# Performance work log

Measured on AMD Instinct MI355X. Metric: run time of the kernel, lower is better.

The kernel has to match this reference:

```python
import jax, jax.numpy as jnp
import numpy as np

H = 64  # hidden_size hardcoded in the module


def _lstm_scan(x_pre, w_hh):
    # x_pre: [T, B, 4H] = x @ W_ih^T + b_ih + b_hh, precomputed for all steps
    # w_hh: [4H, H]. PyTorch gate order: i, f, g, o.
    B = x_pre.shape[1]
    h0 = jnp.zeros((B, H), x_pre.dtype)
    c0 = jnp.zeros((B, H), x_pre.dtype)

    def cell(carry, xp):
        h, c = carry
        gates = xp + h @ w_hh.T  # [B, 4H]
        i, f, g, o = jnp.split(gates, 4, axis=-1)
        i = jax.nn.sigmoid(i)
        f = jax.nn.sigmoid(f)
        g = jnp.tanh(g)
        o = jax.nn.sigmoid(o)
        c = f * c + i * g
        h = o * jnp.tanh(c)
        return (h, c), h

    _, hs = jax.lax.scan(cell, (h0, c0), x_pre)
    return hs  # [T, B, H]


def _bidir_layer(x, w_ih, w_hh, b_ih, b_hh):
    # x: [T, B, D]; w_ih: [2, 4H, D]; w_hh: [2, 4H, H]; b_*: [2, 4H]
    pre_f = jnp.einsum('tbd,gd->tbg', x, w_ih[0]) + b_ih[0] + b_hh[0]
    hs_f = _lstm_scan(pre_f, w_hh[0])
    xr = x[::-1]
    pre_b = jnp.einsum('tbd,gd->tbg', xr, w_ih[1]) + b_ih[1] + b_hh[1]
    hs_b = _lstm_scan(pre_b, w_hh[1])[::-1]  # re-reverse to align with time
    return jnp.concatenate([hs_f, hs_b], axis=-1)  # [T, B, 2H]


def setup_inputs() -> dict:
    key = jax.random.key(0)
    B, T, F = 1024, 512, 32
    ks = jax.random.split(key, 11)
    s = 1.0 / float(np.sqrt(H))  # PyTorch LSTM init: U(-1/sqrt(H), 1/sqrt(H))
    u = lambda k, shape: jax.random.uniform(k, shape, jnp.float32, -s, s)
    return dict(
        x=jax.random.normal(ks[0], (B, T, F), jnp.float32),
        w_ih0=u(ks[1], (2, 4 * H, F)),
        w_hh0=u(ks[2], (2, 4 * H, H)),
        b_ih0=u(ks[3], (2, 4 * H)),
        b_hh0=u(ks[4], (2, 4 * H)),
        w_ih1=u(ks[5], (2, 4 * H, 2 * H)),
        w_hh1=u(ks[6], (2, 4 * H, H)),
        b_ih1=u(ks[7], (2, 4 * H)),
        b_hh1=u(ks[8], (2, 4 * H)),
        fc_w=u(ks[9], (2, 2 * H)),
        fc_b=u(ks[10], (2,)),
    )


def reference(x, w_ih0, w_hh0, b_ih0, b_hh0, w_ih1, w_hh1, b_ih1, b_hh1, fc_w, fc_b):
    xt = jnp.transpose(x, (1, 0, 2))  # [T, B, F]
    h1 = _bidir_layer(xt, w_ih0, w_hh0, b_ih0, b_hh0)  # [T, B, 2H]
    h2 = _bidir_layer(h1, w_ih1, w_hh1, b_ih1, b_hh1)  # [T, B, 2H]
    last = h2[-1]  # out[:, -1, :] in batch_first layout -> [B, 2H]
    return last @ fc_w.T + fc_b  # [B, 2]
```

## Files before the change

kernel.cpp:

```cpp
#include <hip/hip_runtime.h>

#define TT 512
#define BB 1024
#define FF 32
#define HH 64
#define GG 256

__device__ float g_h1[(size_t)BB * TT * 2 * HH];
__device__ float g_pre0[(size_t)2 * BB * TT * GG];
__device__ float g_pre1[(size_t)BB * TT * GG];
__device__ float g_hf[(size_t)BB * HH];

__device__ __forceinline__ float fsigm(float x) {
    float e = __builtin_amdgcn_exp2f(x * -1.44269504088896f);
    return __builtin_amdgcn_rcpf(1.0f + e);
}
__device__ __forceinline__ float ftanh(float x) {
    float e = __builtin_amdgcn_exp2f(x * -2.88539008177793f);
    return 2.0f * __builtin_amdgcn_rcpf(1.0f + e) - 1.0f;
}
__device__ __forceinline__ float rlane(float v, int l) {
    return __int_as_float(__builtin_amdgcn_readlane(__float_as_int(v), l));
}

#define FMA4(c, s, b) do { c.x += (s)*(b).x; c.y += (s)*(b).y; \
                           c.z += (s)*(b).z; c.w += (s)*(b).w; } while (0)

__global__ __launch_bounds__(256, 4) void pre_gemm0(
    const float* __restrict__ x,
    const float* __restrict__ w_ih,
    const float* __restrict__ b_ih,
    const float* __restrict__ b_hh)
{
    const int tid = threadIdx.x;
    const int b   = blockIdx.x >> 1;
    const int dir = blockIdx.x & 1;

    const float4* wsrc = (const float4*)(w_ih + ((size_t)dir * GG + tid) * FF);
    const float4 w0 = wsrc[0], w1 = wsrc[1], w2 = wsrc[2], w3 = wsrc[3],
                 w4 = wsrc[4], w5 = wsrc[5], w6 = wsrc[6], w7 = wsrc[7];
    const float bias = b_ih[dir * GG + tid] + b_hh[dir * GG + tid];

    const float* xb = x + (size_t)b * TT * FF;
    float* ob = g_pre0 + ((size_t)(dir * BB + b) * TT) * GG + tid;

#pragma unroll 2
    for (int t = 0; t < TT; ++t) {
        const float* xp = xb + t * FF;
        float a = bias;
        a += xp[0]  * w0.x + xp[1]  * w0.y + xp[2]  * w0.z + xp[3]  * w0.w;
        a += xp[4]  * w1.x + xp[5]  * w1.y + xp[6]  * w1.z + xp[7]  * w1.w;
        a += xp[8]  * w2.x + xp[9]  * w2.y + xp[10] * w2.z + xp[11] * w2.w;
        a += xp[12] * w3.x + xp[13] * w3.y + xp[14] * w3.z + xp[15] * w3.w;
        a += xp[16] * w4.x + xp[17] * w4.y + xp[18] * w4.z + xp[19] * w4.w;
        a += xp[20] * w5.x + xp[21] * w5.y + xp[22] * w5.z + xp[23] * w5.w;
        a += xp[24] * w6.x + xp[25] * w6.y + xp[26] * w6.z + xp[27] * w6.w;
        a += xp[28] * w7.x + xp[29] * w7.y + xp[30] * w7.z + xp[31] * w7.w;
        ob[(size_t)t * GG] = a;
    }
}

#define PINQ(wq) \
    asm volatile("" : "+v"(wq.x), "+v"(wq.y), "+v"(wq.z), "+v"(wq.w))

template <int L>
__global__ __launch_bounds__(64, 1) void lstm_scan(
    const float* __restrict__ w_hh)
{
    const int l   = threadIdx.x;
    const int dir = (L == 0) ? (blockIdx.x & 1) : 0;
    const int b   = (L == 0) ? (int)(blockIdx.x >> 1) : (int)blockIdx.x;

    const float* wbase = w_hh + (size_t)dir * GG * HH;

    const float4* pi_ = (const float4*)(wbase + (size_t)(0  + l) * HH);
    const float4* pf_ = (const float4*)(wbase + (size_t)(64 + l) * HH);
    float4 wi0 = pi_[0],  wi1 = pi_[1],  wi2 = pi_[2],  wi3 = pi_[3],
           wi4 = pi_[4],  wi5 = pi_[5],  wi6 = pi_[6],  wi7 = pi_[7],
           wi8 = pi_[8],  wi9 = pi_[9],  wi10 = pi_[10], wi11 = pi_[11],
           wi12 = pi_[12], wi13 = pi_[13], wi14 = pi_[14], wi15 = pi_[15];
    float4 wf0 = pf_[0],  wf1 = pf_[1],  wf2 = pf_[2],  wf3 = pf_[3],
           wf4 = pf_[4],  wf5 = pf_[5],  wf6 = pf_[6],  wf7 = pf_[7],
           wf8 = pf_[8],  wf9 = pf_[9],  wf10 = pf_[10], wf11 = pf_[11],
           wf12 = pf_[12], wf13 = pf_[13], wf14 = pf_[14], wf15 = pf_[15];
    PINQ(wi0);  PINQ(wi1);  PINQ(wi2);  PINQ(wi3);
    PINQ(wi4);  PINQ(wi5);  PINQ(wi6);  PINQ(wi7);
    PINQ(wi8);  PINQ(wi9);  PINQ(wi10); PINQ(wi11);
    PINQ(wi12); PINQ(wi13); PINQ(wi14); PINQ(wi15);
    PINQ(wf0);  PINQ(wf1);  PINQ(wf2);  PINQ(wf3);
    PINQ(wf4);  PINQ(wf5);  PINQ(wf6);  PINQ(wf7);
    PINQ(wf8);  PINQ(wf9);  PINQ(wf10); PINQ(wf11);
    PINQ(wf12); PINQ(wf13); PINQ(wf14); PINQ(wf15);

    float4 wg[16], wo[16];
    {
        const float4* pg_ = (const float4*)(wbase + (size_t)(128 + l) * HH);
        const float4* po_ = (const float4*)(wbase + (size_t)(192 + l) * HH);
#pragma unroll
        for (int q = 0; q < 16; ++q) { wg[q] = pg_[q]; wo[q] = po_[q]; }
    }

    const float* pre = (L == 0)
        ? (g_pre0 + ((size_t)(dir * BB + b)) * TT * GG)
        : (g_pre1 + (size_t)b * TT * GG);

    float c = 0.f, h = 0.f;

    const int t0 = dir ? (TT - 1) : 0;
    const int t1 = dir ? (TT - 2) : 1;
    const float* pp0 = pre + (size_t)t0 * GG;
    const float* pp1 = pre + (size_t)t1 * GG;
    float ci0 = pp0[l], cf0 = pp0[64 + l], cg0 = pp0[128 + l], co0 = pp0[192 + l];
    float ci1 = pp1[l], cf1 = pp1[64 + l], cg1 = pp1[128 + l], co1 = pp1[192 + l];

    for (int s = 0; s < TT; ++s) {
        const int t = dir ? (TT - 1 - s) : s;

        float ni = 0.f, nf = 0.f, ng = 0.f, no_ = 0.f;
        if (s + 2 < TT) {
            const int tn = dir ? (TT - 3 - s) : (s + 2);
            const float* np = pre + (size_t)tn * GG;
            ni = np[l]; nf = np[64 + l]; ng = np[128 + l]; no_ = np[192 + l];
        }

        float ai = ci0, af = cf0, ag = cg0, ao = co0;

#define STEPQ(q) do {                                                        \
        float s0 = rlane(h, 4*q+0), s1 = rlane(h, 4*q+1),                    \
              s2 = rlane(h, 4*q+2), s3 = rlane(h, 4*q+3);                    \
        ai += s0*wi##q.x + s1*wi##q.y + s2*wi##q.z + s3*wi##q.w;             \
        af += s0*wf##q.x + s1*wf##q.y + s2*wf##q.z + s3*wf##q.w;             \
        ag += s0*wg[q].x + s1*wg[q].y + s2*wg[q].z + s3*wg[q].w;             \
        ao += s0*wo[q].x + s1*wo[q].y + s2*wo[q].z + s3*wo[q].w;             \
    } while (0)

        STEPQ(0);  STEPQ(1);  STEPQ(2);  STEPQ(3);
        STEPQ(4);  STEPQ(5);  STEPQ(6);  STEPQ(7);
        STEPQ(8);  STEPQ(9);  STEPQ(10); STEPQ(11);
        STEPQ(12); STEPQ(13); STEPQ(14); STEPQ(15);
#undef STEPQ

        const float ig = fsigm(ai);
        const float fg = fsigm(af);
        const float gg = ftanh(ag);
        const float og = fsigm(ao);
        c = fg * c + ig * gg;
        h = og * ftanh(c);

        if (L == 0) {
            g_h1[((size_t)b * TT + t) * (2 * HH) + dir * HH + l] = h;
        } else {
            if (s == TT - 1) g_hf[(size_t)b * HH + l] = h;
        }

        ci0 = ci1; cf0 = cf1; cg0 = cg1; co0 = co1;
        ci1 = ni;  cf1 = nf;  cg1 = ng;  co1 = no_;
    }
}

__global__ __launch_bounds__(256, 2) void pre_gemm1(
    const float* __restrict__ w_ih,
    const float* __restrict__ b_ih,
    const float* __restrict__ b_hh)
{
    __shared__ __align__(16) float As[64 * 132];
    __shared__ __align__(16) float Bs[128 * 68];

    const int tid   = threadIdx.x;
    const int mbase = (int)(blockIdx.x >> 2) * 64;
    const int n0    = (int)(blockIdx.x & 3) * 64;

#pragma unroll
    for (int i = 0; i < 8; ++i) {
        const int qid = tid + 256 * i;
        const int r = qid >> 5, q = qid & 31;
        float4 v = *(const float4*)(g_h1 + (size_t)(mbase + r) * 128 + q * 4);
        *(float4*)(&As[r * 132 + q * 4]) = v;
    }
#pragma unroll
    for (int i = 0; i < 8; ++i) {
        const int qid = tid + 256 * i;
        const int r = qid >> 5, q = qid & 31;
        float4 v = *(const float4*)(w_ih + (size_t)(n0 + r) * 128 + q * 4);
        Bs[(q * 4 + 0) * 68 + r] = v.x;
        Bs[(q * 4 + 1) * 68 + r] = v.y;
        Bs[(q * 4 + 2) * 68 + r] = v.z;
        Bs[(q * 4 + 3) * 68 + r] = v.w;
    }
    __syncthreads();

    const int tx = tid & 15, ty = tid >> 4;

    float4 c0 = make_float4(0.f, 0.f, 0.f, 0.f);
    float4 c1 = c0, c2 = c0, c3 = c0;

#pragma unroll 8
    for (int kq = 0; kq < 32; ++kq) {
        const float4 a0 = *(const float4*)&As[(ty * 4 + 0) * 132 + kq * 4];
        const float4 a1 = *(const float4*)&As[(ty * 4 + 1) * 132 + kq * 4];
        const float4 a2 = *(const float4*)&As[(ty * 4 + 2) * 132 + kq * 4];
        const float4 a3 = *(const float4*)&As[(ty * 4 + 3) * 132 + kq * 4];
        const float4 b0 = *(const float4*)&Bs[(kq * 4 + 0) * 68 + tx * 4];
        const float4 b1 = *(const float4*)&Bs[(kq * 4 + 1) * 68 + tx * 4];
        const float4 b2 = *(const float4*)&Bs[(kq * 4 + 2) * 68 + tx * 4];
        const float4 b3 = *(const float4*)&Bs[(kq * 4 + 3) * 68 + tx * 4];
        FMA4(c0, a0.x, b0); FMA4(c0, a0.y, b1); FMA4(c0, a0.z, b2); FMA4(c0, a0.w, b3);
        FMA4(c1, a1.x, b0); FMA4(c1, a1.y, b1); FMA4(c1, a1.z, b2); FMA4(c1, a1.w, b3);
        FMA4(c2, a2.x, b0); FMA4(c2, a2.y, b1); FMA4(c2, a2.z, b2); FMA4(c2, a2.w, b3);
        FMA4(c3, a3.x, b0); FMA4(c3, a3.y, b1); FMA4(c3, a3.z, b2); FMA4(c3, a3.w, b3);
    }

    float4 bias4;
    bias4.x = b_ih[n0 + tx * 4 + 0] + b_hh[n0 + tx * 4 + 0];
    bias4.y = b_ih[n0 + tx * 4 + 1] + b_hh[n0 + tx * 4 + 1];
    bias4.z = b_ih[n0 + tx * 4 + 2] + b_hh[n0 + tx * 4 + 2];
    bias4.w = b_ih[n0 + tx * 4 + 3] + b_hh[n0 + tx * 4 + 3];

    FMA4(c0, 1.f, bias4); FMA4(c1, 1.f, bias4);
    FMA4(c2, 1.f, bias4); FMA4(c3, 1.f, bias4);

    float* ob = g_pre1 + (size_t)(mbase + ty * 4) * GG + n0 + tx * 4;
    *(float4*)(ob + 0 * (size_t)GG) = c0;
    *(float4*)(ob + 1 * (size_t)GG) = c1;
    *(float4*)(ob + 2 * (size_t)GG) = c2;
    *(float4*)(ob + 3 * (size_t)GG) = c3;
}

#define FMAC4(W, P0, P1, P2, P3, K) do{                                   \
    float4 v_;                                                           \
    v_ = (P0)[K]; acc0 += W.x*v_.x; acc0 += W.y*v_.y; acc0 += W.z*v_.z; acc0 += W.w*v_.w; \
    v_ = (P1)[K]; acc1 += W.x*v_.x; acc1 += W.y*v_.y; acc1 += W.z*v_.z; acc1 += W.w*v_.w; \
    v_ = (P2)[K]; acc2 += W.x*v_.x; acc2 += W.y*v_.y; acc2 += W.z*v_.z; acc2 += W.w*v_.w; \
    v_ = (P3)[K]; acc3 += W.x*v_.x; acc3 += W.y*v_.y; acc3 += W.z*v_.z; acc3 += W.w*v_.w; \
}while(0)

__global__ __launch_bounds__(256, 2) void lstm_final(
    const float* __restrict__ w_ih,
    const float* __restrict__ b_ih,
    const float* __restrict__ b_hh,
    const float* __restrict__ fc_w,
    const float* __restrict__ fc_b,
    float* __restrict__ out)
{
    const int tid = threadIdx.x;
    const int b0  = blockIdx.x * 4;

    __shared__ __align__(16) float x_lds[4][128];
    __shared__ __align__(16) float gact[4][GG];
    __shared__ __align__(16) float last[4][128];

#pragma unroll
    for (int r = 0; r < 2; ++r) {
        int idx = tid + r * 256;
        int b = idx >> 7, col = idx & 127;
        x_lds[b][col] = g_h1[((size_t)(b0 + b) * TT + (TT - 1)) * 128 + col];
    }

    const float4* p = (const float4*)(w_ih + ((size_t)GG + tid) * 128);
    float4 w0 = p[0],  w1 = p[1],  w2 = p[2],  w3 = p[3],  w4 = p[4],  w5 = p[5],
           w6 = p[6],  w7 = p[7],  w8 = p[8],  w9 = p[9],  w10 = p[10], w11 = p[11],
           w12 = p[12], w13 = p[13], w14 = p[14], w15 = p[15], w16 = p[16], w17 = p[17],
           w18 = p[18], w19 = p[19], w20 = p[20], w21 = p[21], w22 = p[22], w23 = p[23],
           w24 = p[24], w25 = p[25], w26 = p[26], w27 = p[27], w28 = p[28], w29 = p[29],
           w30 = p[30], w31 = p[31];
    const float bias = b_ih[GG + tid] + b_hh[GG + tid];
    __syncthreads();

    const float4* xb0 = (const float4*)x_lds[0];
    const float4* xb1 = (const float4*)x_lds[1];
    const float4* xb2 = (const float4*)x_lds[2];
    const float4* xb3 = (const float4*)x_lds[3];

    float acc0 = bias, acc1 = bias, acc2 = bias, acc3 = bias;
    FMAC4(w0, xb0, xb1, xb2, xb3, 0);   FMAC4(w1, xb0, xb1, xb2, xb3, 1);
    FMAC4(w2, xb0, xb1, xb2, xb3, 2);   FMAC4(w3, xb0, xb1, xb2, xb3, 3);
    FMAC4(w4, xb0, xb1, xb2, xb3, 4);   FMAC4(w5, xb0, xb1, xb2, xb3, 5);
    FMAC4(w6, xb0, xb1, xb2, xb3, 6);   FMAC4(w7, xb0, xb1, xb2, xb3, 7);
    FMAC4(w8, xb0, xb1, xb2, xb3, 8);   FMAC4(w9, xb0, xb1, xb2, xb3, 9);
    FMAC4(w10, xb0, xb1, xb2, xb3, 10); FMAC4(w11, xb0, xb1, xb2, xb3, 11);
    FMAC4(w12, xb0, xb1, xb2, xb3, 12); FMAC4(w13, xb0, xb1, xb2, xb3, 13);
    FMAC4(w14, xb0, xb1, xb2, xb3, 14); FMAC4(w15, xb0, xb1, xb2, xb3, 15);
    FMAC4(w16, xb0, xb1, xb2, xb3, 16); FMAC4(w17, xb0, xb1, xb2, xb3, 17);
    FMAC4(w18, xb0, xb1, xb2, xb3, 18); FMAC4(w19, xb0, xb1, xb2, xb3, 19);
    FMAC4(w20, xb0, xb1, xb2, xb3, 20); FMAC4(w21, xb0, xb1, xb2, xb3, 21);
    FMAC4(w22, xb0, xb1, xb2, xb3, 22); FMAC4(w23, xb0, xb1, xb2, xb3, 23);
    FMAC4(w24, xb0, xb1, xb2, xb3, 24); FMAC4(w25, xb0, xb1, xb2, xb3, 25);
    FMAC4(w26, xb0, xb1, xb2, xb3, 26); FMAC4(w27, xb0, xb1, xb2, xb3, 27);
    FMAC4(w28, xb0, xb1, xb2, xb3, 28); FMAC4(w29, xb0, xb1, xb2, xb3, 29);
    FMAC4(w30, xb0, xb1, xb2, xb3, 30); FMAC4(w31, xb0, xb1, xb2, xb3, 31);

    const bool is_g = ((tid >> 6) == 2);
    gact[0][tid] = is_g ? ftanh(acc0) : fsigm(acc0);
    gact[1][tid] = is_g ? ftanh(acc1) : fsigm(acc1);
    gact[2][tid] = is_g ? ftanh(acc2) : fsigm(acc2);
    gact[3][tid] = is_g ? ftanh(acc3) : fsigm(acc3);
    __syncthreads();

    {
        const int cb = tid >> 6, cj = tid & 63;
        float ig = gact[cb][cj];
        float gg = gact[cb][2 * HH + cj];
        float og = gact[cb][3 * HH + cj];
        float c = ig * gg;
        float h = og * ftanh(c);
        last[cb][HH + cj] = h;
        last[cb][cj] = g_hf[(size_t)(b0 + cb) * HH + cj];
    }
    __syncthreads();

    if (tid < 8) {
        int b = tid >> 1, o = tid & 1;
        float a = fc_b[o];
#pragma unroll
        for (int j = 0; j < 128; ++j) a += fc_w[o * 128 + j] * last[b][j];
        out[(size_t)(b0 + b) * 2 + o] = a;
    }
}

extern "C" void kernel_launch(void* const* d_in, const int* in_sizes, int n_in,
                              void* d_out, int out_size, void* d_ws, size_t ws_size,
                              hipStream_t stream) {
    const float* x     = (const float*)d_in[0];
    const float* w_ih0 = (const float*)d_in[1];
    const float* w_hh0 = (const float*)d_in[2];
    const float* b_ih0 = (const float*)d_in[3];
    const float* b_hh0 = (const float*)d_in[4];
    const float* w_ih1 = (const float*)d_in[5];
    const float* w_hh1 = (const float*)d_in[6];
    const float* b_ih1 = (const float*)d_in[7];
    const float* b_hh1 = (const float*)d_in[8];
    const float* fc_w  = (const float*)d_in[9];
    const float* fc_b  = (const float*)d_in[10];
    float* out = (float*)d_out;

    pre_gemm0<<<2048, 256, 0, stream>>>(x, w_ih0, b_ih0, b_hh0);
    lstm_scan<0><<<2048, 64, 0, stream>>>(w_hh0);
    pre_gemm1<<<32768, 256, 0, stream>>>(w_ih1, b_ih1, b_hh1);
    lstm_scan<1><<<1024, 64, 0, stream>>>(w_hh1);
    lstm_final<<<256, 256, 0, stream>>>(w_ih1, b_ih1, b_hh1, fc_w, fc_b, out);
}
```

Before: 2.672 ms.

## Fuse layer-0 input projection into the recurrent scan kernel

Removes the separate pre_gemm0 kernel and its 1 GB intermediate buffer g_pre0. Layer-0 input weights now live in LDS, and each step computes the x@W_ih projection in the scan, broadcasting the x values with readlane. This trades a large HBM write-then-read for extra per-step ALU and LDS reads on the serial critical path. Layer 1's scan is split into its own non-templated kernel with unchanged logic.

Measured after the change: 2.743 ms. 1.03x slower.

```diff
diff --git a/kernel.cpp b/kernel.cpp
--- a/kernel.cpp
+++ b/kernel.cpp
@@ -7,7 +7,6 @@
 #define GG 256
 
 __device__ float g_h1[(size_t)BB * TT * 2 * HH];
-__device__ float g_pre0[(size_t)2 * BB * TT * GG];
 __device__ float g_pre1[(size_t)BB * TT * GG];
 __device__ float g_hf[(size_t)BB * HH];
 
@@ -26,50 +25,37 @@
 #define FMA4(c, s, b) do { c.x += (s)*(b).x; c.y += (s)*(b).y; \
                            c.z += (s)*(b).z; c.w += (s)*(b).w; } while (0)
 
-__global__ __launch_bounds__(256, 4) void pre_gemm0(
+#define PINQ(wq) \
+    asm volatile("" : "+v"(wq.x), "+v"(wq.y), "+v"(wq.z), "+v"(wq.w))
+
+__global__ __launch_bounds__(64, 1) void lstm_scan0(
     const float* __restrict__ x,
     const float* __restrict__ w_ih,
+    const float* __restrict__ w_hh,
     const float* __restrict__ b_ih,
     const float* __restrict__ b_hh)
 {
-    const int tid = threadIdx.x;
-    const int b   = blockIdx.x >> 1;
+    const int l   = threadIdx.x;
     const int dir = blockIdx.x & 1;
-
-    const float4* wsrc = (const float4*)(w_ih + ((size_t)dir * GG + tid) * FF);
-    const float4 w0 = wsrc[0], w1 = wsrc[1], w2 = wsrc[2], w3 = wsrc[3],
-                 w4 = wsrc[4], w5 = wsrc[5], w6 = wsrc[6], w7 = wsrc[7];
-    const float bias = b_ih[dir * GG + tid] + b_hh[dir * GG + tid];
-
-    const float* xb = x + (size_t)b * TT * FF;
-    float* ob = g_pre0 + ((size_t)(dir * BB + b) * TT) * GG + tid;
-
-#pragma unroll 2
-    for (int t = 0; t < TT; ++t) {
-        const float* xp = xb + t * FF;
-        float a = bias;
-        a += xp[0]  * w0.x + xp[1]  * w0.y + xp[2]  * w0.z + xp[3]  * w0.w;
-        a += xp[4]  * w1.x + xp[5]  * w1.y + xp[6]  * w1.z + xp[7]  * w1.w;
-        a += xp[8]  * w2.x + xp[9]  * w2.y + xp[10] * w2.z + xp[11] * w2.w;
-        a += xp[12] * w3.x + xp[13] * w3.y + xp[14] * w3.z + xp[15] * w3.w;
-        a += xp[16] * w4.x + xp[17] * w4.y + xp[18] * w4.z + xp[19] * w4.w;
-        a += xp[20] * w5.x + xp[21] * w5.y + xp[22] * w5.z + xp[23] * w5.w;
-        a += xp[24] * w6.x + xp[25] * w6.y + xp[26] * w6.z + xp[27] * w6.w;
-        a += xp[28] * w7.x + xp[29] * w7.y + xp[30] * w7.z + xp[31] * w7.w;
-        ob[(size_t)t * GG] = a;
-    }
-}
-
-#define PINQ(wq) \
-    asm volatile("" : "+v"(wq.x), "+v"(wq.y), "+v"(wq.z), "+v"(wq.w))
-
-template <int L>
-__global__ __launch_bounds__(64, 1) void lstm_scan(
-    const float* __restrict__ w_hh)
-{
-    const int l   = threadIdx.x;
-    const int dir = (L == 0) ? (blockIdx.x & 1) : 0;
-    const int b   = (L == 0) ? (int)(blockIdx.x >> 1) : (int)blockIdx.x;
+    const int b   = (int)(blockIdx.x >> 1);
+
+    __shared__ __align__(16) float4 wih[4 * 8 * 64];
+    {
+        const float* base = w_ih + (size_t)dir * GG * FF;
+#pragma unroll
+        for (int gc = 0; gc < 4; ++gc) {
+            const float4* src = (const float4*)(base + (size_t)(gc * 64 + l) * FF);
+#pragma unroll
+            for (int q = 0; q < 8; ++q)
+                wih[(gc * 8 + q) * 64 + l] = src[q];
+        }
+    }
+
+    const int gb = dir * GG + l;
+    const float bi = b_ih[gb]            + b_hh[gb];
+    const float bf = b_ih[gb + HH]       + b_hh[gb + HH];
+    const float bg = b_ih[gb + 2 * HH]   + b_hh[gb + 2 * HH];
+    const float bo = b_ih[gb + 3 * HH]   + b_hh[gb + 3 * HH];
 
     const float* wbase = w_hh + (size_t)dir * GG * HH;
 
@@ -100,30 +86,40 @@
         for (int q = 0; q < 16; ++q) { wg[q] = pg_[q]; wo[q] = po_[q]; }
     }
 
-    const float* pre = (L == 0)
-        ? (g_pre0 + ((size_t)(dir * BB + b)) * TT * GG)
-        : (g_pre1 + (size_t)b * TT * GG);
+    __syncthreads();
+
+    const float* xb = x + (size_t)b * TT * FF;
 
     float c = 0.f, h = 0.f;
 
     const int t0 = dir ? (TT - 1) : 0;
     const int t1 = dir ? (TT - 2) : 1;
-    const float* pp0 = pre + (size_t)t0 * GG;
-    const float* pp1 = pre + (size_t)t1 * GG;
-    float ci0 = pp0[l], cf0 = pp0[64 + l], cg0 = pp0[128 + l], co0 = pp0[192 + l];
-    float ci1 = pp1[l], cf1 = pp1[64 + l], cg1 = pp1[128 + l], co1 = pp1[192 + l];
+    float xc = xb[t0 * FF + (l & 31)];
+    float xn = xb[t1 * FF + (l & 31)];
 
     for (int s = 0; s < TT; ++s) {
         const int t = dir ? (TT - 1 - s) : s;
 
-        float ni = 0.f, nf = 0.f, ng = 0.f, no_ = 0.f;
+        float xf = 0.f;
         if (s + 2 < TT) {
             const int tn = dir ? (TT - 3 - s) : (s + 2);
-            const float* np = pre + (size_t)tn * GG;
-            ni = np[l]; nf = np[64 + l]; ng = np[128 + l]; no_ = np[192 + l];
+            xf = xb[tn * FF + (l & 31)];
         }
 
-        float ai = ci0, af = cf0, ag = cg0, ao = co0;
+        float ai = bi, af = bf, ag = bg, ao = bo;
+#pragma unroll
+        for (int q = 0; q < 8; ++q) {
+            const float4 qi = wih[(0 * 8 + q) * 64 + l];
+            const float4 qf = wih[(1 * 8 + q) * 64 + l];
+            const float4 qg = wih[(2 * 8 + q) * 64 + l];
+            const float4 qo = wih[(3 * 8 + q) * 64 + l];
+            const float x0 = rlane(xc, 4 * q + 0), x1 = rlane(xc, 4 * q + 1),
+                        x2 = rlane(xc, 4 * q + 2), x3 = rlane(xc, 4 * q + 3);
+            ai += x0 * qi.x + x1 * qi.y + x2 * qi.z + x3 * qi.w;
+            af += x0 * qf.x + x1 * qf.y + x2 * qf.z + x3 * qf.w;
+            ag += x0 * qg.x + x1 * qg.y + x2 * qg.z + x3 * qg.w;
+            ao += x0 * qo.x + x1 * qo.y + x2 * qo.z + x3 * qo.w;
+        }
 
 #define STEPQ(q) do {                                                        \
         float s0 = rlane(h, 4*q+0), s1 = rlane(h, 4*q+1),                    \
@@ -147,11 +143,88 @@
         c = fg * c + ig * gg;
         h = og * ftanh(c);
 
-        if (L == 0) {
-            g_h1[((size_t)b * TT + t) * (2 * HH) + dir * HH + l] = h;
-        } else {
-            if (s == TT - 1) g_hf[(size_t)b * HH + l] = h;
+        g_h1[((size_t)b * TT + t) * (2 * HH) + dir * HH + l] = h;
+
+        xc = xn; xn = xf;
+    }
+}
+
+__global__ __launch_bounds__(64, 1) void lstm_scan1(
+    const float* __restrict__ w_hh)
+{
+    const int l = threadIdx.x;
+    const int b = (int)blockIdx.x;
+
+    const float* wbase = w_hh;
+
+    const float4* pi_ = (const float4*)(wbase + (size_t)(0  + l) * HH);
+    const float4* pf_ = (const float4*)(wbase + (size_t)(64 + l) * HH);
+    float4 wi0 = pi_[0],  wi1 = pi_[1],  wi2 = pi_[2],  wi3 = pi_[3],
+           wi4 = pi_[4],  wi5 = pi_[5],  wi6 = pi_[6],  wi7 = pi_[7],
+           wi8 = pi_[8],  wi9 = pi_[9],  wi10 = pi_[10], wi11 = pi_[11],
+           wi12 = pi_[12], wi13 = pi_[13], wi14 = pi_[14], wi15 = pi_[15];
+    float4 wf0 = pf_[0],  wf1 = pf_[1],  wf2 = pf_[2],  wf3 = pf_[3],
+           wf4 = pf_[4],  wf5 = pf_[5],  wf6 = pf_[6],  wf7 = pf_[7],
+           wf8 = pf_[8],  wf9 = pf_[9],  wf10 = pf_[10], wf11 = pf_[11],
+           wf12 = pf_[12], wf13 = pf_[13], wf14 = pf_[14], wf15 = pf_[15];
+    PINQ(wi0);  PINQ(wi1);  PINQ(wi2);  PINQ(wi3);
+    PINQ(wi4);  PINQ(wi5);  PINQ(wi6);  PINQ(wi7);
+    PINQ(wi8);  PINQ(wi9);  PINQ(wi10); PINQ(wi11);
+    PINQ(wi12); PINQ(wi13); PINQ(wi14); PINQ(wi15);
+    PINQ(wf0);  PINQ(wf1);  PINQ(wf2);  PINQ(wf3);
+    PINQ(wf4);  PINQ(wf5);  PINQ(wf6);  PINQ(wf7);
+    PINQ(wf8);  PINQ(wf9);  PINQ(wf10); PINQ(wf11);
+    PINQ(wf12); PINQ(wf13); PINQ(wf14); PINQ(wf15);
+
+    float4 wg[16], wo[16];
+    {
+        const float4* pg_ = (const float4*)(wbase + (size_t)(128 + l) * HH);
+        const float4* po_ = (const float4*)(wbase + (size_t)(192 + l) * HH);
+#pragma unroll
+        for (int q = 0; q < 16; ++q) { wg[q] = pg_[q]; wo[q] = po_[q]; }
+    }
+
+    const float* pre = g_pre1 + (size_t)b * TT * GG;
+
+    float c = 0.f, h = 0.f;
+
+    const float* pp0 = pre;
+    const float* pp1 = pre + GG;
+    float ci0 = pp0[l], cf0 = pp0[64 + l], cg0 = pp0[128 + l], co0 = pp0[192 + l];
+    float ci1 = pp1[l], cf1 = pp1[64 + l], cg1 = pp1[128 + l], co1 = pp1[192 + l];
+
+    for (int s = 0; s < TT; ++s) {
+        float ni = 0.f, nf = 0.f, ng = 0.f, no_ = 0.f;
+        if (s + 2 < TT) {
+            const float* np = pre + (size_t)(s + 2) * GG;
+            ni = np[l]; nf = np[64 + l]; ng = np[128 + l]; no_ = np[192 + l];
         }
+
+        float ai = ci0, af = cf0, ag = cg0, ao = co0;
+
+#define STEPQ(q) do {                                                        \
+        float s0 = rlane(h, 4*q+0), s1 = rlane(h, 4*q+1),                    \
+              s2 = rlane(h, 4*q+2), s3 = rlane(h, 4*q+3);                    \
+        ai += s0*wi##q.x + s1*wi##q.y + s2*wi##q.z + s3*wi##q.w;             \
+        af += s0*wf##q.x + s1*wf##q.y + s2*wf##q.z + s3*wf##q.w;             \
+        ag += s0*wg[q].x + s1*wg[q].y + s2*wg[q].z + s3*wg[q].w;             \
+        ao += s0*wo[q].x + s1*wo[q].y + s2*wo[q].z + s3*wo[q].w;             \
+    } while (0)
+
+        STEPQ(0);  STEPQ(1);  STEPQ(2);  STEPQ(3);
+        STEPQ(4);  STEPQ(5);  STEPQ(6);  STEPQ(7);
+        STEPQ(8);  STEPQ(9);  STEPQ(10); STEPQ(11);
+        STEPQ(12); STEPQ(13); STEPQ(14); STEPQ(15);
+#undef STEPQ
+
+        const float ig = fsigm(ai);
+        const float fg = fsigm(af);
+        const float gg = ftanh(ag);
+        const float og = fsigm(ao);
+        c = fg * c + ig * gg;
+        h = og * ftanh(c);
+
+        if (s == TT - 1) g_hf[(size_t)b * HH + l] = h;
 
         ci0 = ci1; cf0 = cf1; cg0 = cg1; co0 = co1;
         ci1 = ni;  cf1 = nf;  cg1 = ng;  co1 = no_;
@@ -333,9 +406,8 @@
     const float* fc_b  = (const float*)d_in[10];
     float* out = (float*)d_out;
 
-    pre_gemm0<<<2048, 256, 0, stream>>>(x, w_ih0, b_ih0, b_hh0);
-    lstm_scan<0><<<2048, 64, 0, stream>>>(w_hh0);
+    lstm_scan0<<<2048, 64, 0, stream>>>(x, w_ih0, w_hh0, b_ih0, b_hh0);
     pre_gemm1<<<32768, 256, 0, stream>>>(w_ih1, b_ih1, b_hh1);
-    lstm_scan<1><<<1024, 64, 0, stream>>>(w_hh1);
+    lstm_scan1<<<1024, 64, 0, stream>>>(w_hh1);
     lstm_final<<<256, 256, 0, stream>>>(w_ih1, b_ih1, b_hh1, fc_w, fc_b, out);
 }
```
